# Performance work log

Hardware: AMD Instinct MI355X
Metric: run time of the kernel (lower is better)

Reference implementation:

```python
import jax, jax.numpy as jnp
import numpy as np

N = 10000      # nodes
E = 320000     # edges
D = 256        # input_nf = output_nf
H = 256        # hidden_nf
ED = 16        # edges_in_d
NORM = 32.0    # normalization_factor


def setup_inputs() -> dict:
    key = jax.random.key(0)
    ks = jax.random.split(key, 16)
    s = 0.02  # param scale
    return {
        "h": jax.random.normal(ks[0], (N, D), dtype=jnp.float32),
        "edge_index": jax.random.randint(ks[1], (2, E), 0, N, dtype=jnp.int64),
        "edge_attr": jax.random.normal(ks[2], (E, ED), dtype=jnp.float32),
        "node_mask": jnp.ones((N, 1), dtype=jnp.float32),
        "edge_mask": jnp.ones((E, 1), dtype=jnp.float32),
        # edge_mlp: Linear(2D+ED -> H), SiLU, Linear(H -> H), SiLU
        "We1": jax.random.normal(ks[3], (2 * D + ED, H), dtype=jnp.float32) * s,
        "be1": jnp.zeros((H,), dtype=jnp.float32),
        "We2": jax.random.normal(ks[4], (H, H), dtype=jnp.float32) * s,
        "be2": jnp.zeros((H,), dtype=jnp.float32),
        # att_mlp: Linear(H -> 1), Sigmoid
        "Wa": jax.random.normal(ks[5], (H, 1), dtype=jnp.float32) * s,
        "ba": jnp.zeros((1,), dtype=jnp.float32),
        # node_mlp: Linear(H + D -> H), SiLU, Linear(H -> D)
        "Wn1": jax.random.normal(ks[6], (H + D, H), dtype=jnp.float32) * s,
        "bn1": jnp.zeros((H,), dtype=jnp.float32),
        "Wn2": jax.random.normal(ks[7], (H, D), dtype=jnp.float32) * s,
        "bn2": jnp.zeros((D,), dtype=jnp.float32),
    }


def reference(h, edge_index, edge_attr, node_mask, edge_mask,
              We1, be1, We2, be2, Wa, ba, Wn1, bn1, Wn2, bn2):
    row, col = edge_index[0], edge_index[1]
    # edge model: gather endpoints, concat with edge_attr -> [E, 2D+ED]
    e_in = jnp.concatenate([h[row], h[col], edge_attr], axis=1)
    mij = jax.nn.silu(jax.nn.silu(e_in @ We1 + be1) @ We2 + be2)  # [E, H]
    att = jax.nn.sigmoid(mij @ Wa + ba)                            # [E, 1]
    edge_feat = mij * att * edge_mask                              # [E, H]
    # node model: scatter-add messages to rows, normalize by constant
    agg = jax.ops.segment_sum(edge_feat, row, num_segments=h.shape[0]) / NORM  # [N, H]
    a = jnp.concatenate([h, agg], axis=1)                          # [N, D+H]
    h_out = h + (jax.nn.silu(a @ Wn1 + bn1) @ Wn2 + bn2)           # residual
    h_out = h_out * node_mask
    return (h_out, mij)
```

## Files before the change

### kernel.cpp

```cpp
#include <hip/hip_runtime.h>

#define NN 10000
#define NE 320000

typedef __bf16 bf16x8 __attribute__((ext_vector_type(8)));
typedef short  s16x8  __attribute__((ext_vector_type(8)));
typedef float  f32x4  __attribute__((ext_vector_type(4)));

__device__ __forceinline__ unsigned short f2bf(float f) {
  return __builtin_bit_cast(unsigned short, (__bf16)f);
}
__device__ __forceinline__ float bf2f(unsigned short s) {
  unsigned u = ((unsigned)s) << 16;
  return __builtin_bit_cast(float, u);
}
__device__ __forceinline__ float sigm(float x) {
  return __builtin_amdgcn_rcpf(1.0f + __expf(-x));
}
__device__ __forceinline__ float silu_f(float x) {
  return x * __builtin_amdgcn_rcpf(1.0f + __expf(-x));
}

__global__ void prep_w(const float* __restrict__ We1, const float* __restrict__ We2,
                       const float* __restrict__ Wn1, const float* __restrict__ Wn2,
                       unsigned short* __restrict__ W1abT, unsigned short* __restrict__ W1cT,
                       unsigned short* __restrict__ We2T,
                       unsigned short* __restrict__ Wn1T, unsigned short* __restrict__ Wn2T) {
  int g = blockIdx.x * blockDim.x + threadIdx.x;
  const int S1 = 512 * 256, S2 = 256 * 32, S3 = 256 * 256, S4 = 256 * 512, S5 = 256 * 256;
  if (g < S1) {
    int n = g >> 8, k = g & 255;
    float v = (n < 256) ? We1[k * 256 + n] : We1[(256 + k) * 256 + (n - 256)];
    W1abT[g] = f2bf(v);
  } else if (g < S1 + S2) {
    int i = g - S1; int n = i >> 5, kk = i & 31;
    float v = (kk < 16) ? We1[(512 + kk) * 256 + n] : 0.0f;
    W1cT[i] = f2bf(v);
  } else if (g < S1 + S2 + S3) {
    int i = g - S1 - S2; int n = i >> 8, k = i & 255;
    We2T[i] = f2bf(We2[k * 256 + n]);
  } else if (g < S1 + S2 + S3 + S4) {
    int i = g - S1 - S2 - S3; int n = i >> 9, k = i & 511;
    Wn1T[i] = f2bf(Wn1[k * 256 + n]);
  } else if (g < S1 + S2 + S3 + S4 + S5) {
    int i = g - S1 - S2 - S3 - S4; int n = i >> 8, k = i & 255;
    Wn2T[i] = f2bf(Wn2[k * 256 + n]);
  }
}

__global__ void prep_x(const float* __restrict__ h, unsigned short* __restrict__ hb) {
  int g = blockIdx.x * blockDim.x + threadIdx.x;
  if (g < NN * 64) {
    float4 f = ((const float4*)h)[g];
    unsigned short* d = hb + g * 4;
    d[0] = f2bf(f.x); d[1] = f2bf(f.y); d[2] = f2bf(f.z); d[3] = f2bf(f.w);
  }
}

__global__ void hist_kernel(const int* __restrict__ eidx, int* __restrict__ rowi,
                            int* __restrict__ counts) {
  __shared__ int s64;
  if (threadIdx.x == 0) {
    bool b = true;
    for (int i = 1; i < 64; i += 2) b = b && (eidx[i] == 0);
    s64 = b ? 1 : 0;
  }
  __syncthreads();
  int e = blockIdx.x * 256 + threadIdx.x;
  if (e < NE) {
    int r = s64 ? (int)((const long long*)eidx)[e] : eidx[e];
    rowi[e] = r;
    atomicAdd(&counts[r], 1);
  }
}

__global__ __launch_bounds__(1024) void scan_kernel(const int* __restrict__ counts,
                                                    int* __restrict__ rowStart,
                                                    int* __restrict__ cursor) {
  __shared__ int part[1024];
  int t = threadIdx.x;
  int local[10];
  int s = 0;
  #pragma unroll
  for (int i = 0; i < 10; i++) {
    int idx = t * 10 + i;
    int c = (idx < NN) ? counts[idx] : 0;
    local[i] = s; s += c;
  }
  part[t] = s;
  __syncthreads();
  int val = s;
  for (int off = 1; off < 1024; off <<= 1) {
    int tmp = (t >= off) ? part[t - off] : 0;
    __syncthreads();
    part[t] += tmp;
    __syncthreads();
  }
  int base = part[t] - val;
  #pragma unroll
  for (int i = 0; i < 10; i++) {
    int idx = t * 10 + i;
    if (idx < NN) { int v = base + local[i]; rowStart[idx] = v; cursor[idx] = v; }
  }
  if (t == 1023) rowStart[NN] = NE;
}

__global__ void scatter_kernel(const int* __restrict__ rowi, int* __restrict__ cursor,
                               int* __restrict__ eorder, int* __restrict__ rowSorted) {
  int e = blockIdx.x * 256 + threadIdx.x;
  if (e < NE) {
    int r = rowi[e];
    int pos = atomicAdd(&cursor[r], 1);
    eorder[pos] = e;
    rowSorted[pos] = r;
  }
}

__global__ __launch_bounds__(512, 4) void hpq_kernel(
    const unsigned short* __restrict__ hb, const unsigned short* __restrict__ W1abT,
    unsigned short* __restrict__ hPQb) {
  __shared__ unsigned short Abuf[128 * 40];

  const int tid = threadIdx.x;
  const int lane = tid & 63;
  const int wid = tid >> 6;
  const int wrr = wid >> 2, wcc = wid & 3;
  const int n0 = blockIdx.x * 128;
  const int coh = blockIdx.y;
  const unsigned short* Bsrc = W1abT + ((size_t)(coh << 8)) * 256;

  f32x4 acc[4][4];
  #pragma unroll
  for (int m = 0; m < 4; m++)
    #pragma unroll
    for (int n = 0; n < 4; n++) acc[m][n] = (f32x4){0.f, 0.f, 0.f, 0.f};

  const int eA = tid >> 2, sA = tid & 3;
  int nodeA = n0 + eA; if (nodeA >= NN) nodeA = NN - 1;
  const int rbase = (wrr << 6) + (lane & 15);
  const int koff = (lane >> 4) << 3;
  const int cfrag = lane & 15;

  for (int kt = 0; kt < 8; ++kt) {
    const int k0 = kt << 5;
    __syncthreads();
    *(s16x8*)&Abuf[eA * 40 + (sA << 3)] = *(const s16x8*)(hb + (size_t)nodeA * 256 + k0 + (sA << 3));
    __syncthreads();
    bf16x8 a[4], b[4];
    #pragma unroll
    for (int m = 0; m < 4; m++)
      a[m] = __builtin_bit_cast(bf16x8, *(const s16x8*)&Abuf[(rbase + m * 16) * 40 + koff]);
    #pragma unroll
    for (int n = 0; n < 4; n++)
      b[n] = __builtin_bit_cast(bf16x8,
               *(const s16x8*)(Bsrc + (((wcc << 6) + n * 16 + cfrag) << 8) + k0 + koff));
    #pragma unroll
    for (int m = 0; m < 4; m++)
      #pragma unroll
      for (int n = 0; n < 4; n++)
        acc[m][n] = __builtin_amdgcn_mfma_f32_16x16x32_bf16(a[m], b[n], acc[m][n], 0, 0, 0);
  }

  #pragma unroll
  for (int m = 0; m < 4; m++) {
    int rl = (wrr << 6) + m * 16 + ((lane >> 4) << 2);
    #pragma unroll
    for (int n = 0; n < 4; n++) {
      int cg = (wcc << 6) + n * 16 + cfrag;
      #pragma unroll
      for (int j = 0; j < 4; j++) {
        int rg = n0 + rl + j;
        if (rg < NN) hPQb[(size_t)rg * 512 + (coh << 8) + cg] = f2bf(acc[m][n][j]);
      }
    }
  }
}

__global__ __launch_bounds__(512, 4) void edge_kernel(
    const unsigned short* __restrict__ hPQb, const int* __restrict__ eidx,
    const float* __restrict__ eattr, const float* __restrict__ emask,
    const unsigned short* __restrict__ W1cT, const float* __restrict__ be1,
    const unsigned short* __restrict__ We2T, const float* __restrict__ be2,
    const float* __restrict__ Wa, const float* __restrict__ ba,
    const int* __restrict__ eorder, const int* __restrict__ rowSorted,
    float* __restrict__ mij_out, float* __restrict__ agg) {
  __shared__ unsigned short A2[128 * 264];
  __shared__ float attP[4][128];
  __shared__ float attL[128];
  __shared__ int rowL[128], colL[128], origL[128];
  __shared__ float waL[256], be1L[256], be2L[256];
  __shared__ int s64;

  const int tid = threadIdx.x;
  const int lane = tid & 63;
  const int wid = tid >> 6;
  const int wr = wid >> 2, wc = wid & 3;
  const int nwg = NE / 128, q = nwg >> 3, r = nwg & 7;
  const int xcd = blockIdx.x & 7, bi = blockIdx.x >> 3;
  const int wg = (xcd < r ? xcd * (q + 1) : r * (q + 1) + (xcd - r) * q) + bi;
  const int e0 = wg * 128;
  const int cfrag = lane & 15;
  const int lq = lane >> 4;
  const int koff = lq << 3;
  const int rbase = (wr << 6) + cfrag;

  if (tid == 0) {
    bool b = true;
    for (int i = 1; i < 64; i += 2) b = b && (eidx[i] == 0);
    s64 = b ? 1 : 0;
  }
  __syncthreads();

  if (tid < 128) {
    int orig = eorder[e0 + tid];
    origL[tid] = orig;
    rowL[tid] = rowSorted[e0 + tid];
    colL[tid] = s64 ? (int)((const long long*)eidx)[NE + orig] : eidx[NE + orig];
  }
  if (tid >= 256) {
    int i = tid - 256;
    waL[i] = Wa[i]; be1L[i] = be1[i]; be2L[i] = be2[i];
  }
  __syncthreads();

  f32x4 acc[4][4];
  #pragma unroll
  for (int m = 0; m < 4; m++)
    #pragma unroll
    for (int n = 0; n < 4; n++) acc[m][n] = (f32x4){0.f, 0.f, 0.f, 0.f};

  {
    int e = tid >> 2, p = tid & 3;
    int c0 = p << 6;
    const unsigned short* pr = hPQb + (size_t)rowL[e] * 512 + c0;
    const unsigned short* pc = hPQb + (size_t)colL[e] * 512 + 256 + c0;
    #pragma unroll
    for (int qq = 0; qq < 8; ++qq) {
      s16x8 vr = *(const s16x8*)(pr + (qq << 3));
      s16x8 vc = *(const s16x8*)(pc + (qq << 3));
      s16x8 vo;
      #pragma unroll
      for (int j = 0; j < 8; ++j)
        vo[j] = (short)f2bf(bf2f((unsigned short)vr[j]) + bf2f((unsigned short)vc[j]));
      *(s16x8*)&A2[e * 264 + c0 + (qq << 3)] = vo;
    }
  }
  {
    bf16x8 a[4], b[4];
    #pragma unroll
    for (int m = 0; m < 4; m++) {
      int rl = rbase + m * 16;
      if (koff < 16) {
        const float* src = eattr + (size_t)origL[rl] * 16 + koff;
        float4 f0 = *(const float4*)src;
        float4 f1 = *(const float4*)(src + 4);
        s16x8 v;
        v[0] = (short)f2bf(f0.x); v[1] = (short)f2bf(f0.y);
        v[2] = (short)f2bf(f0.z); v[3] = (short)f2bf(f0.w);
        v[4] = (short)f2bf(f1.x); v[5] = (short)f2bf(f1.y);
        v[6] = (short)f2bf(f1.z); v[7] = (short)f2bf(f1.w);
        a[m] = __builtin_bit_cast(bf16x8, v);
      } else {
        a[m] = __builtin_bit_cast(bf16x8, (s16x8){0, 0, 0, 0, 0, 0, 0, 0});
      }
    }
    #pragma unroll
    for (int n = 0; n < 4; n++)
      b[n] = __builtin_bit_cast(bf16x8,
               *(const s16x8*)(W1cT + (((wc << 6) + n * 16 + cfrag) << 5) + koff));
    #pragma unroll
    for (int m = 0; m < 4; m++)
      #pragma unroll
      for (int n = 0; n < 4; n++)
        acc[m][n] = __builtin_amdgcn_mfma_f32_16x16x32_bf16(a[m], b[n], acc[m][n], 0, 0, 0);
  }
  __syncthreads();

  #pragma unroll
  for (int m = 0; m < 4; m++) {
    int rl = (wr << 6) + m * 16 + (lq << 2);
    #pragma unroll
    for (int n = 0; n < 4; n++) {
      int cg = (wc << 6) + n * 16 + cfrag;
      float bias = be1L[cg];
      #pragma unroll
      for (int j = 0; j < 4; j++) {
        float x = acc[m][n][j] + bf2f(A2[(rl + j) * 264 + cg]) + bias;
        A2[(rl + j) * 264 + cg] = f2bf(silu_f(x));
      }
      acc[m][n] = (f32x4){0.f, 0.f, 0.f, 0.f};
    }
  }
  __syncthreads();

  #pragma unroll
  for (int t = 0; t < 8; ++t) {
    const int k0 = t << 5;
    bf16x8 a[4], b[4];
    #pragma unroll
    for (int m = 0; m < 4; m++)
      a[m] = __builtin_bit_cast(bf16x8, *(const s16x8*)&A2[(rbase + m * 16) * 264 + k0 + koff]);
    #pragma unroll
    for (int n = 0; n < 4; n++)
      b[n] = __builtin_bit_cast(bf16x8,
               *(const s16x8*)(We2T + (((wc << 6) + n * 16 + cfrag) << 8) + k0 + koff));
    #pragma unroll
    for (int m = 0; m < 4; m++)
      #pragma unroll
      for (int n = 0; n < 4; n++)
        acc[m][n] = __builtin_amdgcn_mfma_f32_16x16x32_bf16(a[m], b[n], acc[m][n], 0, 0, 0);
  }
  __syncthreads();

  float part[4][4];
  #pragma unroll
  for (int m = 0; m < 4; m++)
    #pragma unroll
    for (int j = 0; j < 4; j++) part[m][j] = 0.f;

  #pragma unroll
  for (int m = 0; m < 4; m++) {
    #pragma unroll
    for (int n = 0; n < 4; n++) {
      int cg = (wc << 6) + n * 16 + cfrag;
      float bias = be2L[cg];
      float wav = waL[cg];
      #pragma unroll
      for (int j = 0; j < 4; j++) {
        int row = (wr << 6) + m * 16 + (lq << 2) + j;
        float x = silu_f(acc[m][n][j] + bias);
        mij_out[(size_t)origL[row] * 256 + cg] = x;
        A2[row * 264 + cg] = f2bf(x);
        part[m][j] += x * wav;
      }
    }
  }
  #pragma unroll
  for (int m = 0; m < 4; m++)
    #pragma unroll
    for (int j = 0; j < 4; j++) {
      float p = part[m][j];
      p += __shfl_xor(p, 1);
      p += __shfl_xor(p, 2);
      p += __shfl_xor(p, 4);
      p += __shfl_xor(p, 8);
      part[m][j] = p;
    }
  if (cfrag == 0) {
    #pragma unroll
    for (int m = 0; m < 4; m++)
      #pragma unroll
      for (int j = 0; j < 4; j++)
        attP[wc][(wr << 6) + m * 16 + (lq << 2) + j] = part[m][j];
  }
  __syncthreads();
  if (tid < 128) {
    float s = attP[0][tid] + attP[1][tid] + attP[2][tid] + attP[3][tid] + ba[0];
    attL[tid] = sigm(s) * emask[origL[tid]];
  }
  __syncthreads();

  {
    const int half = tid >> 8;
    const int c = tid & 255;
    const int i0 = half << 6, i1 = i0 + 64;
    const int fd = rowL[i0];
    float acc2 = 0.f;
    int prev = fd;
    for (int i = i0; i < i1; ++i) {
      int rr = rowL[i];
      if (rr != prev) {
        if (prev == fd) atomicAdd(&agg[(size_t)prev * 256 + c], acc2);
        else            agg[(size_t)prev * 256 + c] = acc2;
        acc2 = 0.f; prev = rr;
      }
      acc2 += attL[i] * bf2f(A2[i * 264 + c]);
    }
    atomicAdd(&agg[(size_t)prev * 256 + c], acc2);
  }
}

__global__ __launch_bounds__(512, 4) void node_kernel(
    const float* __restrict__ h, const float* __restrict__ agg,
    const float* __restrict__ nmask,
    const unsigned short* __restrict__ Wn1T, const float* __restrict__ bn1,
    const unsigned short* __restrict__ Wn2T, const float* __restrict__ bn2,
    float* __restrict__ hout) {
  __shared__ unsigned short Abuf[128 * 40];
  __shared__ unsigned short A2[128 * 264];
  __shared__ float bn1L[256], bn2L[256];

  const int tid = threadIdx.x;
  const int lane = tid & 63;
  const int wid = tid >> 6;
  const int n0 = blockIdx.x * 128;

  if (tid < 256) { bn1L[tid] = bn1[tid]; bn2L[tid] = bn2[tid]; }

  f32x4 acc[4][4];
  #pragma unroll
  for (int m = 0; m < 4; m++)
    #pragma unroll
    for (int n = 0; n < 4; n++) acc[m][n] = (f32x4){0.f, 0.f, 0.f, 0.f};

  const int eA = tid >> 2, sA = tid & 3;
  int nodeA = n0 + eA; if (nodeA >= NN) nodeA = NN - 1;
  const int wrr = wid >> 2, wcc = wid & 3;
  const int rbase = (wrr << 6) + (lane & 15);
  const int koff = (lane >> 4) << 3;
  const int cfrag = lane & 15;

  for (int kt = 0; kt < 16; ++kt) {
    const int k0 = kt << 5;
    __syncthreads();
    {
      const float* src = (k0 < 256) ? (h + (size_t)nodeA * 256 + k0 + (sA << 3))
                                    : (agg + (size_t)nodeA * 256 + (k0 - 256) + (sA << 3));
      const float sc = (k0 < 256) ? 1.0f : (1.0f / 32.0f);
      float4 f0 = *(const float4*)src;
      float4 f1 = *(const float4*)(src + 4);
      s16x8 v;
      v[0] = (short)f2bf(f0.x * sc); v[1] = (short)f2bf(f0.y * sc);
      v[2] = (short)f2bf(f0.z * sc); v[3] = (short)f2bf(f0.w * sc);
      v[4] = (short)f2bf(f1.x * sc); v[5] = (short)f2bf(f1.y * sc);
      v[6] = (short)f2bf(f1.z * sc); v[7] = (short)f2bf(f1.w * sc);
      *(s16x8*)&Abuf[eA * 40 + (sA << 3)] = v;
    }
    __syncthreads();
    bf16x8 a[4], b[4];
    #pragma unroll
    for (int m = 0; m < 4; m++)
      a[m] = __builtin_bit_cast(bf16x8, *(const s16x8*)&Abuf[(rbase + m * 16) * 40 + koff]);
    #pragma unroll
    for (int n = 0; n < 4; n++)
      b[n] = __builtin_bit_cast(bf16x8,
               *(const s16x8*)(Wn1T + (((wcc << 6) + n * 16 + cfrag) << 9) + k0 + koff));
    #pragma unroll
    for (int m = 0; m < 4; m++)
      #pragma unroll
      for (int n = 0; n < 4; n++)
        acc[m][n] = __builtin_amdgcn_mfma_f32_16x16x32_bf16(a[m], b[n], acc[m][n], 0, 0, 0);
  }

  #pragma unroll
  for (int m = 0; m < 4; m++) {
    int rl = (wrr << 6) + m * 16 + ((lane >> 4) << 2);
    #pragma unroll
    for (int n = 0; n < 4; n++) {
      int cg = (wcc << 6) + n * 16 + cfrag;
      float bias = bn1L[cg];
      #pragma unroll
      for (int j = 0; j < 4; j++) {
        float x = acc[m][n][j] + bias;
        A2[(rl + j) * 264 + cg] = f2bf(silu_f(x));
      }
      acc[m][n] = (f32x4){0.f, 0.f, 0.f, 0.f};
    }
  }
  __syncthreads();

  #pragma unroll
  for (int kt = 0; kt < 8; ++kt) {
    const int k0 = kt << 5;
    bf16x8 a[4], b[4];
    #pragma unroll
    for (int m = 0; m < 4; m++)
      a[m] = __builtin_bit_cast(bf16x8, *(const s16x8*)&A2[(rbase + m * 16) * 264 + k0 + koff]);
    #pragma unroll
    for (int n = 0; n < 4; n++)
      b[n] = __builtin_bit_cast(bf16x8,
               *(const s16x8*)(Wn2T + (((wcc << 6) + n * 16 + cfrag) << 8) + k0 + koff));
    #pragma unroll
    for (int m = 0; m < 4; m++)
      #pragma unroll
      for (int n = 0; n < 4; n++)
        acc[m][n] = __builtin_amdgcn_mfma_f32_16x16x32_bf16(a[m], b[n], acc[m][n], 0, 0, 0);
  }

  #pragma unroll
  for (int m = 0; m < 4; m++) {
    int rl = (wrr << 6) + m * 16 + ((lane >> 4) << 2);
    #pragma unroll
    for (int n = 0; n < 4; n++) {
      int cg = (wcc << 6) + n * 16 + cfrag;
      #pragma unroll
      for (int j = 0; j < 4; j++) {
        int rg = n0 + rl + j;
        if (rg < NN) {
          float val = acc[m][n][j] + bn2L[cg];
          float o = (h[(size_t)rg * 256 + cg] + val) * nmask[rg];
          hout[(size_t)rg * 256 + cg] = o;
        }
      }
    }
  }
}

extern "C" void kernel_launch(void* const* d_in, const int* in_sizes, int n_in,
                              void* d_out, int out_size, void* d_ws, size_t ws_size,
                              hipStream_t stream) {
  (void)in_sizes; (void)n_in; (void)out_size; (void)ws_size;
  const float* h     = (const float*)d_in[0];
  const int*   eidx  = (const int*)d_in[1];
  const float* eattr = (const float*)d_in[2];
  const float* nmask = (const float*)d_in[3];
  const float* emask = (const float*)d_in[4];
  const float* We1 = (const float*)d_in[5];
  const float* be1 = (const float*)d_in[6];
  const float* We2 = (const float*)d_in[7];
  const float* be2 = (const float*)d_in[8];
  const float* Wa  = (const float*)d_in[9];
  const float* ba  = (const float*)d_in[10];
  const float* Wn1 = (const float*)d_in[11];
  const float* bn1 = (const float*)d_in[12];
  const float* Wn2 = (const float*)d_in[13];
  const float* bn2 = (const float*)d_in[14];

  char* ws = (char*)d_ws;
  unsigned short* W1abT = (unsigned short*)(ws + 0);
  unsigned short* W1cT  = (unsigned short*)(ws + 262144);
  unsigned short* We2T  = (unsigned short*)(ws + 278528);
  unsigned short* Wn1T  = (unsigned short*)(ws + 409600);
  unsigned short* Wn2T  = (unsigned short*)(ws + 671744);
  unsigned short* hPQb  = (unsigned short*)(ws + 802816);
  float* agg      = (float*)(ws + 11042816);
  int*   counts   = (int*)(ws + 21282816);
  int*   rowStart = (int*)(ws + 21322816);
  int*   cursor   = (int*)(ws + 21362824);
  int*   eorder   = (int*)(ws + 21402824);
  int*   rowi     = (int*)(ws + 22682824);
  int*   rowSorted= (int*)(ws + 23962824);
  unsigned short* hb = (unsigned short*)(ws + 25242824);

  float* hout = (float*)d_out;
  float* mij  = (float*)d_out + (size_t)NN * 256;

  hipMemsetAsync(counts, 0, NN * sizeof(int), stream);
  hipMemsetAsync(agg, 0, (size_t)NN * 256 * sizeof(float), stream);
  prep_w<<<1568, 256, 0, stream>>>(We1, We2, Wn1, Wn2, W1abT, W1cT, We2T, Wn1T, Wn2T);
  prep_x<<<2500, 256, 0, stream>>>(h, hb);
  hist_kernel<<<(NE + 255) / 256, 256, 0, stream>>>(eidx, rowi, counts);
  scan_kernel<<<1, 1024, 0, stream>>>(counts, rowStart, cursor);
  scatter_kernel<<<(NE + 255) / 256, 256, 0, stream>>>(rowi, cursor, eorder, rowSorted);
  hpq_kernel<<<dim3((NN + 127) / 128, 2), 512, 0, stream>>>(hb, W1abT, hPQb);
  edge_kernel<<<NE / 128, 512, 0, stream>>>(hPQb, eidx, eattr, emask, W1cT, be1, We2T, be2,
                                            Wa, ba, eorder, rowSorted, mij, agg);
  node_kernel<<<(NN + 127) / 128, 512, 0, stream>>>(h, agg, nmask, Wn1T, bn1, Wn2T, bn2, hout);
}
```

Baseline: 361.1 us.

## Merge prep kernels, presort col indices, drop LDS staging in GEMMs, prefetch We2

Fuses weight conversion, h-to-bf16 conversion and the row histogram into one launch, cutting kernel launches. The scatter kernel now writes column indices in sorted order, so the edge kernel loads them contiguously instead of gathering through eorder. The hpq and node kernels load A fragments straight from global memory, removing the LDS staging buffer and its barriers. The node kernel reads the bf16 copy of h, and the edge kernel prefetches the first two We2 k-tiles into registers before a barrier. The trade-off is more uncoalesced global loads and higher register pressure.

```diff
diff --git a/kernel.cpp b/kernel.cpp
--- a/kernel.cpp
+++ b/kernel.cpp
@@ -21,55 +21,50 @@
   return x * __builtin_amdgcn_rcpf(1.0f + __expf(-x));
 }
 
-__global__ void prep_w(const float* __restrict__ We1, const float* __restrict__ We2,
-                       const float* __restrict__ Wn1, const float* __restrict__ Wn2,
-                       unsigned short* __restrict__ W1abT, unsigned short* __restrict__ W1cT,
-                       unsigned short* __restrict__ We2T,
-                       unsigned short* __restrict__ Wn1T, unsigned short* __restrict__ Wn2T) {
-  int g = blockIdx.x * blockDim.x + threadIdx.x;
-  const int S1 = 512 * 256, S2 = 256 * 32, S3 = 256 * 256, S4 = 256 * 512, S5 = 256 * 256;
-  if (g < S1) {
-    int n = g >> 8, k = g & 255;
-    float v = (n < 256) ? We1[k * 256 + n] : We1[(256 + k) * 256 + (n - 256)];
-    W1abT[g] = f2bf(v);
-  } else if (g < S1 + S2) {
-    int i = g - S1; int n = i >> 5, kk = i & 31;
-    float v = (kk < 16) ? We1[(512 + kk) * 256 + n] : 0.0f;
-    W1cT[i] = f2bf(v);
-  } else if (g < S1 + S2 + S3) {
-    int i = g - S1 - S2; int n = i >> 8, k = i & 255;
-    We2T[i] = f2bf(We2[k * 256 + n]);
-  } else if (g < S1 + S2 + S3 + S4) {
-    int i = g - S1 - S2 - S3; int n = i >> 9, k = i & 511;
-    Wn1T[i] = f2bf(Wn1[k * 256 + n]);
-  } else if (g < S1 + S2 + S3 + S4 + S5) {
-    int i = g - S1 - S2 - S3 - S4; int n = i >> 8, k = i & 255;
-    Wn2T[i] = f2bf(Wn2[k * 256 + n]);
-  }
-}
-
-__global__ void prep_x(const float* __restrict__ h, unsigned short* __restrict__ hb) {
-  int g = blockIdx.x * blockDim.x + threadIdx.x;
-  if (g < NN * 64) {
+__global__ void prep_all(const float* __restrict__ We1, const float* __restrict__ We2,
+                         const float* __restrict__ Wn1, const float* __restrict__ Wn2,
+                         const float* __restrict__ h, const int* __restrict__ eidx,
+                         unsigned short* __restrict__ W1abT, unsigned short* __restrict__ W1cT,
+                         unsigned short* __restrict__ We2T,
+                         unsigned short* __restrict__ Wn1T, unsigned short* __restrict__ Wn2T,
+                         unsigned short* __restrict__ hb, int* __restrict__ counts) {
+  const int b = blockIdx.x;
+  if (b < 1568) {
+    int g = b * 256 + threadIdx.x;
+    const int S1 = 512 * 256, S2 = 256 * 32, S3 = 256 * 256, S4 = 256 * 512, S5 = 256 * 256;
+    if (g < S1) {
+      int n = g >> 8, k = g & 255;
+      float v = (n < 256) ? We1[k * 256 + n] : We1[(256 + k) * 256 + (n - 256)];
+      W1abT[g] = f2bf(v);
+    } else if (g < S1 + S2) {
+      int i = g - S1; int n = i >> 5, kk = i & 31;
+      float v = (kk < 16) ? We1[(512 + kk) * 256 + n] : 0.0f;
+      W1cT[i] = f2bf(v);
+    } else if (g < S1 + S2 + S3) {
+      int i = g - S1 - S2; int n = i >> 8, k = i & 255;
+      We2T[i] = f2bf(We2[k * 256 + n]);
+    } else if (g < S1 + S2 + S3 + S4) {
+      int i = g - S1 - S2 - S3; int n = i >> 9, k = i & 511;
+      Wn1T[i] = f2bf(Wn1[k * 256 + n]);
+    } else if (g < S1 + S2 + S3 + S4 + S5) {
+      int i = g - S1 - S2 - S3 - S4; int n = i >> 8, k = i & 255;
+      Wn2T[i] = f2bf(Wn2[k * 256 + n]);
+    }
+  } else if (b < 4068) {
+    int g = (b - 1568) * 256 + threadIdx.x;
     float4 f = ((const float4*)h)[g];
     unsigned short* d = hb + g * 4;
     d[0] = f2bf(f.x); d[1] = f2bf(f.y); d[2] = f2bf(f.z); d[3] = f2bf(f.w);
-  }
-}
-
-__global__ void hist_kernel(const int* __restrict__ eidx, int* __restrict__ rowi,
-                            int* __restrict__ counts) {
-  __shared__ int s64;
-  if (threadIdx.x == 0) {
-    bool b = true;
-    for (int i = 1; i < 64; i += 2) b = b && (eidx[i] == 0);
-    s64 = b ? 1 : 0;
-  }
-  __syncthreads();
-  int e = blockIdx.x * 256 + threadIdx.x;
-  if (e < NE) {
+  } else {
+    __shared__ int s64;
+    if (threadIdx.x == 0) {
+      bool bb = true;
+      for (int i = 1; i < 64; i += 2) bb = bb && (eidx[i] == 0);
+      s64 = bb ? 1 : 0;
+    }
+    __syncthreads();
+    int e = (b - 4068) * 256 + threadIdx.x;
     int r = s64 ? (int)((const long long*)eidx)[e] : eidx[e];
-    rowi[e] = r;
     atomicAdd(&counts[r], 1);
   }
 }
@@ -105,22 +100,35 @@
   if (t == 1023) rowStart[NN] = NE;
 }
 
-__global__ void scatter_kernel(const int* __restrict__ rowi, int* __restrict__ cursor,
-                               int* __restrict__ eorder, int* __restrict__ rowSorted) {
+__global__ void scatter_kernel(const int* __restrict__ eidx, int* __restrict__ cursor,
+                               int* __restrict__ eorder, int* __restrict__ rowSorted,
+                               int* __restrict__ colSorted) {
+  __shared__ int s64;
+  if (threadIdx.x == 0) {
+    bool bb = true;
+    for (int i = 1; i < 64; i += 2) bb = bb && (eidx[i] == 0);
+    s64 = bb ? 1 : 0;
+  }
+  __syncthreads();
   int e = blockIdx.x * 256 + threadIdx.x;
   if (e < NE) {
-    int r = rowi[e];
+    int r, c;
+    if (s64) {
+      const long long* p64 = (const long long*)eidx;
+      r = (int)p64[e]; c = (int)p64[NE + e];
+    } else {
+      r = eidx[e]; c = eidx[NE + e];
+    }
     int pos = atomicAdd(&cursor[r], 1);
     eorder[pos] = e;
     rowSorted[pos] = r;
+    colSorted[pos] = c;
   }
 }
 
 __global__ __launch_bounds__(512, 4) void hpq_kernel(
     const unsigned short* __restrict__ hb, const unsigned short* __restrict__ W1abT,
     unsigned short* __restrict__ hPQb) {
-  __shared__ unsigned short Abuf[128 * 40];
-
   const int tid = threadIdx.x;
   const int lane = tid & 63;
   const int wid = tid >> 6;
@@ -135,21 +143,23 @@
     #pragma unroll
     for (int n = 0; n < 4; n++) acc[m][n] = (f32x4){0.f, 0.f, 0.f, 0.f};
 
-  const int eA = tid >> 2, sA = tid & 3;
-  int nodeA = n0 + eA; if (nodeA >= NN) nodeA = NN - 1;
   const int rbase = (wrr << 6) + (lane & 15);
   const int koff = (lane >> 4) << 3;
   const int cfrag = lane & 15;
 
+  int rg[4];
+  #pragma unroll
+  for (int m = 0; m < 4; m++) {
+    rg[m] = n0 + rbase + m * 16; if (rg[m] >= NN) rg[m] = NN - 1;
+  }
+
+  #pragma unroll
   for (int kt = 0; kt < 8; ++kt) {
     const int k0 = kt << 5;
-    __syncthreads();
-    *(s16x8*)&Abuf[eA * 40 + (sA << 3)] = *(const s16x8*)(hb + (size_t)nodeA * 256 + k0 + (sA << 3));
-    __syncthreads();
     bf16x8 a[4], b[4];
     #pragma unroll
     for (int m = 0; m < 4; m++)
-      a[m] = __builtin_bit_cast(bf16x8, *(const s16x8*)&Abuf[(rbase + m * 16) * 40 + koff]);
+      a[m] = __builtin_bit_cast(bf16x8, *(const s16x8*)(hb + (size_t)rg[m] * 256 + k0 + koff));
     #pragma unroll
     for (int n = 0; n < 4; n++)
       b[n] = __builtin_bit_cast(bf16x8,
@@ -169,15 +179,15 @@
       int cg = (wcc << 6) + n * 16 + cfrag;
       #pragma unroll
       for (int j = 0; j < 4; j++) {
-        int rg = n0 + rl + j;
-        if (rg < NN) hPQb[(size_t)rg * 512 + (coh << 8) + cg] = f2bf(acc[m][n][j]);
+        int rr = n0 + rl + j;
+        if (rr < NN) hPQb[(size_t)rr * 512 + (coh << 8) + cg] = f2bf(acc[m][n][j]);
       }
     }
   }
 }
 
 __global__ __launch_bounds__(512, 4) void edge_kernel(
-    const unsigned short* __restrict__ hPQb, const int* __restrict__ eidx,
+    const unsigned short* __restrict__ hPQb, const int* __restrict__ colSorted,
     const float* __restrict__ eattr, const float* __restrict__ emask,
     const unsigned short* __restrict__ W1cT, const float* __restrict__ be1,
     const unsigned short* __restrict__ We2T, const float* __restrict__ be2,
@@ -189,7 +199,6 @@
   __shared__ float attL[128];
   __shared__ int rowL[128], colL[128], origL[128];
   __shared__ float waL[256], be1L[256], be2L[256];
-  __shared__ int s64;
 
   const int tid = threadIdx.x;
   const int lane = tid & 63;
@@ -204,18 +213,10 @@
   const int koff = lq << 3;
   const int rbase = (wr << 6) + cfrag;
 
-  if (tid == 0) {
-    bool b = true;
-    for (int i = 1; i < 64; i += 2) b = b && (eidx[i] == 0);
-    s64 = b ? 1 : 0;
-  }
-  __syncthreads();
-
   if (tid < 128) {
-    int orig = eorder[e0 + tid];
-    origL[tid] = orig;
+    origL[tid] = eorder[e0 + tid];
     rowL[tid] = rowSorted[e0 + tid];
-    colL[tid] = s64 ? (int)((const long long*)eidx)[NE + orig] : eidx[NE + orig];
+    colL[tid] = colSorted[e0 + tid];
   }
   if (tid >= 256) {
     int i = tid - 256;
@@ -274,6 +275,14 @@
       for (int n = 0; n < 4; n++)
         acc[m][n] = __builtin_amdgcn_mfma_f32_16x16x32_bf16(a[m], b[n], acc[m][n], 0, 0, 0);
   }
+
+  s16x8 bpre0[4], bpre1[4];
+  #pragma unroll
+  for (int n = 0; n < 4; n++) {
+    const unsigned short* base = We2T + (((wc << 6) + n * 16 + cfrag) << 8) + koff;
+    bpre0[n] = *(const s16x8*)(base);
+    bpre1[n] = *(const s16x8*)(base + 32);
+  }
   __syncthreads();
 
   #pragma unroll
@@ -301,9 +310,12 @@
     for (int m = 0; m < 4; m++)
       a[m] = __builtin_bit_cast(bf16x8, *(const s16x8*)&A2[(rbase + m * 16) * 264 + k0 + koff]);
     #pragma unroll
-    for (int n = 0; n < 4; n++)
-      b[n] = __builtin_bit_cast(bf16x8,
-               *(const s16x8*)(We2T + (((wc << 6) + n * 16 + cfrag) << 8) + k0 + koff));
+    for (int n = 0; n < 4; n++) {
+      if (t == 0)      b[n] = __builtin_bit_cast(bf16x8, bpre0[n]);
+      else if (t == 1) b[n] = __builtin_bit_cast(bf16x8, bpre1[n]);
+      else             b[n] = __builtin_bit_cast(bf16x8,
+                         *(const s16x8*)(We2T + (((wc << 6) + n * 16 + cfrag) << 8) + k0 + koff));
+    }
     #pragma unroll
     for (int m = 0; m < 4; m++)
       #pragma unroll
@@ -381,12 +393,11 @@
 }
 
 __global__ __launch_bounds__(512, 4) void node_kernel(
-    const float* __restrict__ h, const float* __restrict__ agg,
-    const float* __restrict__ nmask,
+    const float* __restrict__ h, const unsigned short* __restrict__ hb,
+    const float* __restrict__ agg, const float* __restrict__ nmask,
     const unsigned short* __restrict__ Wn1T, const float* __restrict__ bn1,
     const unsigned short* __restrict__ Wn2T, const float* __restrict__ bn2,
     float* __restrict__ hout) {
-  __shared__ unsigned short Abuf[128 * 40];
   __shared__ unsigned short A2[128 * 264];
   __shared__ float bn1L[256], bn2L[256];
 
@@ -403,38 +414,54 @@
     #pragma unroll
     for (int n = 0; n < 4; n++) acc[m][n] = (f32x4){0.f, 0.f, 0.f, 0.f};
 
-  const int eA = tid >> 2, sA = tid & 3;
-  int nodeA = n0 + eA; if (nodeA >= NN) nodeA = NN - 1;
   const int wrr = wid >> 2, wcc = wid & 3;
   const int rbase = (wrr << 6) + (lane & 15);
   const int koff = (lane >> 4) << 3;
   const int cfrag = lane & 15;
 
-  for (int kt = 0; kt < 16; ++kt) {
+  int rg[4];
+  #pragma unroll
+  for (int m = 0; m < 4; m++) {
+    rg[m] = n0 + rbase + m * 16; if (rg[m] >= NN) rg[m] = NN - 1;
+  }
+
+  #pragma unroll
+  for (int kt = 0; kt < 8; ++kt) {
     const int k0 = kt << 5;
-    __syncthreads();
-    {
-      const float* src = (k0 < 256) ? (h + (size_t)nodeA * 256 + k0 + (sA << 3))
-                                    : (agg + (size_t)nodeA * 256 + (k0 - 256) + (sA << 3));
-      const float sc = (k0 < 256) ? 1.0f : (1.0f / 32.0f);
+    bf16x8 a[4], b[4];
+    #pragma unroll
+    for (int m = 0; m < 4; m++)
+      a[m] = __builtin_bit_cast(bf16x8, *(const s16x8*)(hb + (size_t)rg[m] * 256 + k0 + koff));
+    #pragma unroll
+    for (int n = 0; n < 4; n++)
+      b[n] = __builtin_bit_cast(bf16x8,
+               *(const s16x8*)(Wn1T + (((wcc << 6) + n * 16 + cfrag) << 9) + k0 + koff));
+    #pragma unroll
+    for (int m = 0; m < 4; m++)
+      #pragma unroll
+      for (int n = 0; n < 4; n++)
+        acc[m][n] = __builtin_amdgcn_mfma_f32_16x16x32_bf16(a[m], b[n], acc[m][n], 0, 0, 0);
+  }
+  #pragma unroll
+  for (int kt = 0; kt < 8; ++kt) {
+    const int k0 = kt << 5;
+    bf16x8 a[4], b[4];
+    #pragma unroll
+    for (int m = 0; m < 4; m++) {
+      const float* src = agg + (size_t)rg[m] * 256 + k0 + koff;
       float4 f0 = *(const float4*)src;
       float4 f1 = *(const float4*)(src + 4);
       s16x8 v;
-      v[0] = (short)f2bf(f0.x * sc); v[1] = (short)f2bf(f0.y * sc);
-      v[2] = (short)f2bf(f0.z * sc); v[3] = (short)f2bf(f0.w * sc);
-      v[4] = (short)f2bf(f1.x * sc); v[5] = (short)f2bf(f1.y * sc);
-      v[6] = (short)f2bf(f1.z * sc); v[7] = (short)f2bf(f1.w * sc);
-      *(s16x8*)&Abuf[eA * 40 + (sA << 3)] = v;
-    }
-    __syncthreads();
-    bf16x8 a[4], b[4];
-    #pragma unroll
-    for (int m = 0; m < 4; m++)
-      a[m] = __builtin_bit_cast(bf16x8, *(const s16x8*)&Abuf[(rbase + m * 16) * 40 + koff]);
+      v[0] = (short)f2bf(f0.x * 0.03125f); v[1] = (short)f2bf(f0.y * 0.03125f);
+      v[2] = (short)f2bf(f0.z * 0.03125f); v[3] = (short)f2bf(f0.w * 0.03125f);
+      v[4] = (short)f2bf(f1.x * 0.03125f); v[5] = (short)f2bf(f1.y * 0.03125f);
+      v[6] = (short)f2bf(f1.z * 0.03125f); v[7] = (short)f2bf(f1.w * 0.03125f);
+      a[m] = __builtin_bit_cast(bf16x8, v);
+    }
     #pragma unroll
     for (int n = 0; n < 4; n++)
       b[n] = __builtin_bit_cast(bf16x8,
-               *(const s16x8*)(Wn1T + (((wcc << 6) + n * 16 + cfrag) << 9) + k0 + koff));
+               *(const s16x8*)(Wn1T + (((wcc << 6) + n * 16 + cfrag) << 9) + 256 + k0 + koff));
     #pragma unroll
     for (int m = 0; m < 4; m++)
       #pragma unroll
@@ -485,11 +512,11 @@
       int cg = (wcc << 6) + n * 16 + cfrag;
       #pragma unroll
       for (int j = 0; j < 4; j++) {
-        int rg = n0 + rl + j;
-        if (rg < NN) {
+        int rr = n0 + rl + j;
+        if (rr < NN) {
           float val = acc[m][n][j] + bn2L[cg];
-          float o = (h[(size_t)rg * 256 + cg] + val) * nmask[rg];
-          hout[(size_t)rg * 256 + cg] = o;
+          float o = (h[(size_t)rr * 256 + cg] + val) * nmask[rr];
+          hout[(size_t)rr * 256 + cg] = o;
         }
       }
     }
@@ -528,7 +555,7 @@
   int*   rowStart = (int*)(ws + 21322816);
   int*   cursor   = (int*)(ws + 21362824);
   int*   eorder   = (int*)(ws + 21402824);
-  int*   rowi     = (int*)(ws + 22682824);
+  int*   colSorted= (int*)(ws + 22682824);
   int*   rowSorted= (int*)(ws + 23962824);
   unsigned short* hb = (unsigned short*)(ws + 25242824);
 
@@ -537,13 +564,12 @@
 
   hipMemsetAsync(counts, 0, NN * sizeof(int), stream);
   hipMemsetAsync(agg, 0, (size_t)NN * 256 * sizeof(float), stream);
-  prep_w<<<1568, 256, 0, stream>>>(We1, We2, Wn1, Wn2, W1abT, W1cT, We2T, Wn1T, Wn2T);
-  prep_x<<<2500, 256, 0, stream>>>(h, hb);
-  hist_kernel<<<(NE + 255) / 256, 256, 0, stream>>>(eidx, rowi, counts);
+  prep_all<<<5318, 256, 0, stream>>>(We1, We2, Wn1, Wn2, h, eidx,
+                                     W1abT, W1cT, We2T, Wn1T, Wn2T, hb, counts);
   scan_kernel<<<1, 1024, 0, stream>>>(counts, rowStart, cursor);
-  scatter_kernel<<<(NE + 255) / 256, 256, 0, stream>>>(rowi, cursor, eorder, rowSorted);
+  scatter_kernel<<<(NE + 255) / 256, 256, 0, stream>>>(eidx, cursor, eorder, rowSorted, colSorted);
   hpq_kernel<<<dim3((NN + 127) / 128, 2), 512, 0, stream>>>(hb, W1abT, hPQb);
-  edge_kernel<<<NE / 128, 512, 0, stream>>>(hPQb, eidx, eattr, emask, W1cT, be1, We2T, be2,
+  edge_kernel<<<NE / 128, 512, 0, stream>>>(hPQb, colSorted, eattr, emask, W1cT, be1, We2T, be2,
                                             Wa, ba, eorder, rowSorted, mij, agg);
-  node_kernel<<<(NN + 127) / 128, 512, 0, stream>>>(h, agg, nmask, Wn1T, bn1, Wn2T, bn2, hout);
-}
+  node_kernel<<<(NN + 127) / 128, 512, 0, stream>>>(h, hb, agg, nmask, Wn1T, bn1, Wn2T, bn2, hout);
+}
```

After: 402.4 us. +11.4%, slower.
